# Kernel optimization log

Measured on AMD Instinct MI355X. Metric: run time of the kernel, lower is better.

The kernel has to match this reference:

```python
import jax, jax.numpy as jnp
import numpy as np

CHANNELS = 96


def make_sharpen_kernel(channels: int) -> jnp.ndarray:
    # (C_out, C_in, 3, 3), block-diagonal: per-channel 3x3 sharpen stencil
    k = jnp.full((3, 3), -0.1, dtype=jnp.float32).at[1, 1].set(1.8)
    eye = jnp.eye(channels, dtype=jnp.float32)  # (C, C)
    return eye[:, :, None, None] * k[None, None, :, :]


def setup_inputs() -> dict:
    key = jax.random.key(0)
    x = jax.random.normal(key, (16, CHANNELS, 256, 256), dtype=jnp.float32)
    kernel = make_sharpen_kernel(CHANNELS)
    return {"x": x, "kernel": kernel}


def reference(x, kernel):
    # Faithful to F.conv2d(x, kernel, stride=1, padding=1) with the dense
    # (block-diagonal) kernel the torch module constructs.
    return jax.lax.conv_general_dilated(
        x, kernel,
        window_strides=(1, 1),
        padding=((1, 1), (1, 1)),
        dimension_numbers=("NCHW", "OIHW", "NCHW"),
    )
```

## Files before the change

kernel.cpp:

```cpp
#include <hip/hip_runtime.h>

#define CHN 96
#define IMG_H 256
#define IMG_W 256
#define ROWS_PER_BLOCK 8

__global__ __launch_bounds__(ROWS_PER_BLOCK * 64)
void sharpen3x3_dw(const float* __restrict__ x,
                   const float* __restrict__ kern,
                   float* __restrict__ out)
{
    const int lane = threadIdx.x & 63;
    const int wave = threadIdx.x >> 6;

    const int groups_per_img = IMG_H / ROWS_PER_BLOCK;
    const int img  = blockIdx.x / groups_per_img;
    const int grp  = blockIdx.x % groups_per_img;
    const int c    = img % CHN;
    const int y    = grp * ROWS_PER_BLOCK + wave;

    const float* kw = kern + ((size_t)c * CHN + c) * 9;
    float w0 = kw[0], w1 = kw[1], w2 = kw[2];
    float w3 = kw[3], w4 = kw[4], w5 = kw[5];
    float w6 = kw[6], w7 = kw[7], w8 = kw[8];

    const float* xplane = x + (size_t)img * IMG_H * IMG_W;

    float acc0 = 0.f, acc1 = 0.f, acc2 = 0.f, acc3 = 0.f;

    #pragma unroll
    for (int ky = 0; ky < 3; ++ky) {
        const int yy = y + ky - 1;
        float4 v = make_float4(0.f, 0.f, 0.f, 0.f);
        if (yy >= 0 && yy < IMG_H) {
            v = *(const float4*)(xplane + (size_t)yy * IMG_W + 4 * lane);
        }
        float l = __shfl_up(v.w, 1);
        float r = __shfl_down(v.x, 1);
        if (lane == 0)  l = 0.f;
        if (lane == 63) r = 0.f;

        float ka, kb, kc;
        if      (ky == 0) { ka = w0; kb = w1; kc = w2; }
        else if (ky == 1) { ka = w3; kb = w4; kc = w5; }
        else              { ka = w6; kb = w7; kc = w8; }

        acc0 += ka * l   + kb * v.x + kc * v.y;
        acc1 += ka * v.x + kb * v.y + kc * v.z;
        acc2 += ka * v.y + kb * v.z + kc * v.w;
        acc3 += ka * v.z + kb * v.w + kc * r;
    }

    float4 o = make_float4(acc0, acc1, acc2, acc3);
    *(float4*)(out + ((size_t)img * IMG_H + y) * IMG_W + 4 * lane) = o;
}

extern "C" void kernel_launch(void* const* d_in, const int* in_sizes, int n_in,
                              void* d_out, int out_size, void* d_ws, size_t ws_size,
                              hipStream_t stream) {
    const float* x    = (const float*)d_in[0];
    const float* kern = (const float*)d_in[1];
    float* out        = (float*)d_out;

    const int n_imgs = 16 * CHN;
    const int grid   = n_imgs * (IMG_H / ROWS_PER_BLOCK);

    hipLaunchKernelGGL(sharpen3x3_dw, dim3(grid), dim3(ROWS_PER_BLOCK * 64),
                       0, stream, x, kern, out);
}
```

Baseline: 164.3 us.

## Stream rows down 64-row strips per wave with register row reuse

Each wave now walks a 64-row vertical strip, keeping the previous two rows in registers and loading four new rows per iteration, so each input row is read about once instead of three times. Outputs are written with nontemporal stores to avoid polluting cache. The grid shrinks to far fewer blocks, which reduces parallelism and puts serial dependence within each wave.

After: 158.9 us. 1.03x faster.

```diff
diff --git a/kernel.cpp b/kernel.cpp
--- a/kernel.cpp
+++ b/kernel.cpp
@@ -3,56 +3,110 @@
 #define CHN 96
 #define IMG_H 256
 #define IMG_W 256
-#define ROWS_PER_BLOCK 8
+#define STRIP 64
+#define WPB 8
 
-__global__ __launch_bounds__(ROWS_PER_BLOCK * 64)
-void sharpen3x3_dw(const float* __restrict__ x,
-                   const float* __restrict__ kern,
-                   float* __restrict__ out)
+typedef float vfloat4 __attribute__((ext_vector_type(4)));
+
+struct Row { float l, x, y, z, w, r; };
+
+__device__ __forceinline__ Row mkrow(vfloat4 v, int lane) {
+    Row r;
+    r.x = v.x; r.y = v.y; r.z = v.z; r.w = v.w;
+    r.l = __shfl_up(v.w, 1);
+    r.r = __shfl_down(v.x, 1);
+    if (lane == 0)  r.l = 0.f;
+    if (lane == 63) r.r = 0.f;
+    return r;
+}
+
+__device__ __forceinline__ vfloat4 stencil(const Row& a, const Row& b, const Row& c,
+                                           float w0, float w1, float w2,
+                                           float w3, float w4, float w5,
+                                           float w6, float w7, float w8) {
+    vfloat4 o;
+    o.x = w0*a.l + w1*a.x + w2*a.y
+        + w3*b.l + w4*b.x + w5*b.y
+        + w6*c.l + w7*c.x + w8*c.y;
+    o.y = w0*a.x + w1*a.y + w2*a.z
+        + w3*b.x + w4*b.y + w5*b.z
+        + w6*c.x + w7*c.y + w8*c.z;
+    o.z = w0*a.y + w1*a.z + w2*a.w
+        + w3*b.y + w4*b.z + w5*b.w
+        + w6*c.y + w7*c.z + w8*c.w;
+    o.w = w0*a.z + w1*a.w + w2*a.r
+        + w3*b.z + w4*b.w + w5*b.r
+        + w6*c.z + w7*c.w + w8*c.r;
+    return o;
+}
+
+__global__ __launch_bounds__(WPB * 64)
+void sharpen3x3_strip(const float* __restrict__ x,
+                      const float* __restrict__ kern,
+                      float* __restrict__ out)
 {
     const int lane = threadIdx.x & 63;
     const int wave = threadIdx.x >> 6;
 
-    const int groups_per_img = IMG_H / ROWS_PER_BLOCK;
-    const int img  = blockIdx.x / groups_per_img;
-    const int grp  = blockIdx.x % groups_per_img;
-    const int c    = img % CHN;
-    const int y    = grp * ROWS_PER_BLOCK + wave;
+    const int strip_id = blockIdx.x * WPB + wave;
+    const int spp      = IMG_H / STRIP;
+    const int plane    = strip_id / spp;
+    const int sy       = (strip_id % spp) * STRIP;
+    const int c        = plane % CHN;
 
     const float* kw = kern + ((size_t)c * CHN + c) * 9;
-    float w0 = kw[0], w1 = kw[1], w2 = kw[2];
-    float w3 = kw[3], w4 = kw[4], w5 = kw[5];
-    float w6 = kw[6], w7 = kw[7], w8 = kw[8];
+    const float w0 = kw[0], w1 = kw[1], w2 = kw[2];
+    const float w3 = kw[3], w4 = kw[4], w5 = kw[5];
+    const float w6 = kw[6], w7 = kw[7], w8 = kw[8];
 
-    const float* xplane = x + (size_t)img * IMG_H * IMG_W;
+    const float* xp = x   + (size_t)plane * IMG_H * IMG_W;
+    float*       op = out + (size_t)plane * IMG_H * IMG_W;
 
-    float acc0 = 0.f, acc1 = 0.f, acc2 = 0.f, acc3 = 0.f;
+    const int col = 4 * lane;
 
-    #pragma unroll
-    for (int ky = 0; ky < 3; ++ky) {
-        const int yy = y + ky - 1;
-        float4 v = make_float4(0.f, 0.f, 0.f, 0.f);
-        if (yy >= 0 && yy < IMG_H) {
-            v = *(const float4*)(xplane + (size_t)yy * IMG_W + 4 * lane);
-        }
-        float l = __shfl_up(v.w, 1);
-        float r = __shfl_down(v.x, 1);
-        if (lane == 0)  l = 0.f;
-        if (lane == 63) r = 0.f;
-
-        float ka, kb, kc;
-        if      (ky == 0) { ka = w0; kb = w1; kc = w2; }
-        else if (ky == 1) { ka = w3; kb = w4; kc = w5; }
-        else              { ka = w6; kb = w7; kc = w8; }
-
-        acc0 += ka * l   + kb * v.x + kc * v.y;
-        acc1 += ka * v.x + kb * v.y + kc * v.z;
-        acc2 += ka * v.y + kb * v.z + kc * v.w;
-        acc3 += ka * v.z + kb * v.w + kc * r;
+    Row prev, cur;
+    if (sy == 0) {
+        prev = Row{0.f, 0.f, 0.f, 0.f, 0.f, 0.f};
+    } else {
+        vfloat4 vp = *(const vfloat4*)(xp + (size_t)(sy - 1) * IMG_W + col);
+        prev = mkrow(vp, lane);
+    }
+    {
+        vfloat4 vc = *(const vfloat4*)(xp + (size_t)sy * IMG_W + col);
+        cur = mkrow(vc, lane);
     }
 
-    float4 o = make_float4(acc0, acc1, acc2, acc3);
-    *(float4*)(out + ((size_t)img * IMG_H + y) * IMG_W + 4 * lane) = o;
+    for (int i = 0; i < STRIP; i += 4) {
+        const int y = sy + i;
+        const float* base = xp + (size_t)(y + 1) * IMG_W + col;
+
+        vfloat4 v0 = *(const vfloat4*)(base);
+        vfloat4 v1 = *(const vfloat4*)(base + IMG_W);
+        vfloat4 v2 = *(const vfloat4*)(base + 2 * IMG_W);
+        vfloat4 v3;
+        const bool last = (y + 4 >= IMG_H);
+        if (!last) v3 = *(const vfloat4*)(base + 3 * IMG_W);
+        else       v3 = (vfloat4){0.f, 0.f, 0.f, 0.f};
+
+        Row n0 = mkrow(v0, lane);
+        Row n1 = mkrow(v1, lane);
+        Row n2 = mkrow(v2, lane);
+        Row n3 = last ? Row{0.f,0.f,0.f,0.f,0.f,0.f} : mkrow(v3, lane);
+
+        vfloat4 o0 = stencil(prev, cur, n0, w0,w1,w2,w3,w4,w5,w6,w7,w8);
+        vfloat4 o1 = stencil(cur,  n0,  n1, w0,w1,w2,w3,w4,w5,w6,w7,w8);
+        vfloat4 o2 = stencil(n0,   n1,  n2, w0,w1,w2,w3,w4,w5,w6,w7,w8);
+        vfloat4 o3 = stencil(n1,   n2,  n3, w0,w1,w2,w3,w4,w5,w6,w7,w8);
+
+        float* ob = op + (size_t)y * IMG_W + col;
+        __builtin_nontemporal_store(o0, (vfloat4*)(ob));
+        __builtin_nontemporal_store(o1, (vfloat4*)(ob + IMG_W));
+        __builtin_nontemporal_store(o2, (vfloat4*)(ob + 2 * IMG_W));
+        __builtin_nontemporal_store(o3, (vfloat4*)(ob + 3 * IMG_W));
+
+        prev = n2;
+        cur  = n3;
+    }
 }
 
 extern "C" void kernel_launch(void* const* d_in, const int* in_sizes, int n_in,
@@ -62,9 +116,9 @@
     const float* kern = (const float*)d_in[1];
     float* out        = (float*)d_out;
 
-    const int n_imgs = 16 * CHN;
-    const int grid   = n_imgs * (IMG_H / ROWS_PER_BLOCK);
+    const int n_strips = 16 * CHN * (IMG_H / STRIP);
+    const int grid     = n_strips / WPB;
 
-    hipLaunchKernelGGL(sharpen3x3_dw, dim3(grid), dim3(ROWS_PER_BLOCK * 64),
+    hipLaunchKernelGGL(sharpen3x3_strip, dim3(grid), dim3(WPB * 64),
                        0, stream, x, kern, out);
 }
```
